# Kernel tuning notes

Hardware: AMD Instinct MI355X
Metric: run time of the kernel (lower is better)

## Reference

```python
import jax, jax.numpy as jnp
import numpy as np

B, S, QS, KS, F, H = 4, 2048, 512, 1024, 1024, 16
DH = F // H  # head dim = 64


def setup_inputs() -> dict:
    key = jax.random.key(0)
    ks = jax.random.split(key, 7)
    s = 0.02
    return {
        "x": jax.random.normal(ks[0], (B, S, QS), dtype=jnp.float32),
        "y": jax.random.normal(ks[1], (B, S, QS), dtype=jnp.float32),
        "z": jax.random.normal(ks[2], (B, S, KS), dtype=jnp.float32),
        "Wq": jax.random.normal(ks[3], (2 * QS, F), dtype=jnp.float32) * s,
        "Wk": jax.random.normal(ks[4], (KS, F), dtype=jnp.float32) * s,
        "Wv": jax.random.normal(ks[5], (KS, F), dtype=jnp.float32) * s,
        "Wo": jax.random.normal(ks[6], (F, F), dtype=jnp.float32) * s,
    }


def _split_heads(t):
    # [B, S, F] -> [B, H, S, DH]
    return t.reshape(B, S, H, DH).transpose(0, 2, 1, 3)


def reference(x, y, z, Wq, Wk, Wv, Wo):
    q = _split_heads(jnp.concatenate([x, y], axis=-1) @ Wq)  # [B,H,S,DH]
    k = _split_heads(z @ Wk)
    v = _split_heads(z @ Wv)
    scale = 1.0 / jnp.sqrt(jnp.asarray(DH, dtype=q.dtype))
    scores = jnp.einsum("bhsd,bhtd->bhst", q, k) * scale  # [B,H,S,S]
    attn = jax.nn.softmax(scores, axis=-1)
    out = jnp.einsum("bhst,bhtd->bhsd", attn, v)  # [B,H,S,DH]
    out = out.transpose(0, 2, 1, 3).reshape(B, S, F)
    return out @ Wo
```

## Files before the change

### kernel.cpp

```cpp
#include <hip/hip_runtime.h>

typedef __attribute__((ext_vector_type(8))) short short8;
typedef __attribute__((ext_vector_type(4))) float f32x4;
typedef __attribute__((ext_vector_type(16))) float f32x16;
typedef __attribute__((ext_vector_type(4))) unsigned short us4;
typedef __attribute__((ext_vector_type(4))) unsigned int u32x4;

#define GLOAD16(gsrc, ldst)                                             \
  __builtin_amdgcn_global_load_lds(                                     \
      (const __attribute__((address_space(1))) unsigned int*)(gsrc),    \
      (__attribute__((address_space(3))) unsigned int*)(ldst), 16, 0, 0)

#define VMEM_DRAIN_BARRIER()                              \
  do {                                                    \
    asm volatile("s_waitcnt vmcnt(0)" ::: "memory");      \
    __builtin_amdgcn_sched_barrier(0);                    \
    __syncthreads();                                      \
  } while (0)

#if __has_builtin(__builtin_amdgcn_exp2f)
#define EXP2F(x) __builtin_amdgcn_exp2f(x)
#else
#define EXP2F(x) exp2f(x)
#endif

static __device__ __forceinline__ unsigned short f2bf(float f) {
  unsigned int u = __float_as_uint(f);
  u += 0x7fffu + ((u >> 16) & 1u);
  return (unsigned short)(u >> 16);
}

static __device__ __forceinline__ unsigned cvtpk(float lo, float hi) {
  unsigned r;
  asm("v_cvt_pk_bf16_f32 %0, %1, %2" : "=v"(r) : "v"(lo), "v"(hi));
  return r;
}

__global__ __launch_bounds__(256) void prep(const float* __restrict__ x,
                                            const float* __restrict__ y,
                                            const float* __restrict__ z,
                                            const float* __restrict__ Wq,
                                            const float* __restrict__ Wk,
                                            const float* __restrict__ Wv,
                                            const float* __restrict__ Wo,
                                            unsigned short* __restrict__ XY,
                                            unsigned short* __restrict__ Z,
                                            unsigned short* __restrict__ WqT,
                                            unsigned short* __restrict__ WkT,
                                            unsigned short* __restrict__ WvT,
                                            unsigned short* __restrict__ WoT) {
  __shared__ __align__(16) unsigned short LT[64 * 72];
  const int bid = blockIdx.x, t = threadIdx.x;

  if (bid < 2048) {
    const int NX = (8192 * 512) / 4;
    const int NZ = (8192 * 1024) / 4;
    const int total = 2 * NX + NZ;
    for (int idx = bid * 256 + t; idx < total; idx += 2048 * 256) {
      const float* src;
      unsigned short* dst;
      if (idx < NX) {
        int p = idx * 4; int row = p >> 9, c = p & 511;
        src = x + p; dst = XY + (size_t)row * 1024 + c;
      } else if (idx < 2 * NX) {
        int p = (idx - NX) * 4; int row = p >> 9, c = p & 511;
        src = y + p; dst = XY + (size_t)row * 1024 + 512 + c;
      } else {
        int p = (idx - 2 * NX) * 4;
        src = z + p; dst = Z + p;
      }
      float4 v = *(const float4*)src;
      us4 o; o[0] = f2bf(v.x); o[1] = f2bf(v.y); o[2] = f2bf(v.z); o[3] = f2bf(v.w);
      *(us4*)dst = o;
    }
    return;
  }

  const int seg = (bid - 2048) >> 8;
  const int local = (bid - 2048) & 255;
  const float* W = (seg == 0) ? Wq : (seg == 1) ? Wk : (seg == 2) ? Wv : Wo;
  unsigned short* WT = (seg == 0) ? WqT : (seg == 1) ? WkT : (seg == 2) ? WvT : WoT;
  const int k0 = (local >> 4) * 64, n0 = (local & 15) * 64;
#pragma unroll
  for (int j = 0; j < 4; ++j) {
    int r = j * 16 + (t >> 4);
    int c = (t & 15) * 4;
    float4 w = *(const float4*)(W + (size_t)(k0 + r) * 1024 + n0 + c);
    LT[(c + 0) * 72 + r] = f2bf(w.x);
    LT[(c + 1) * 72 + r] = f2bf(w.y);
    LT[(c + 2) * 72 + r] = f2bf(w.z);
    LT[(c + 3) * 72 + r] = f2bf(w.w);
  }
  __syncthreads();
#pragma unroll
  for (int j = 0; j < 2; ++j) {
    int n = j * 32 + (t >> 3), ch = t & 7;
    *(short8*)(WT + (size_t)(n0 + n) * 1024 + k0 + ch * 8) =
        *(const short8*)(LT + n * 72 + ch * 8);
  }
}

__global__ __launch_bounds__(256) void qkv_gemm(const unsigned short* __restrict__ XY,
                                                const unsigned short* __restrict__ Zb,
                                                const unsigned short* __restrict__ WqT,
                                                const unsigned short* __restrict__ WkT,
                                                const unsigned short* __restrict__ WvT,
                                                unsigned short* __restrict__ Qb,
                                                unsigned short* __restrict__ Kb,
                                                unsigned short* __restrict__ Vb) {
  __shared__ __align__(16) unsigned short As[128 * 32];
  __shared__ __align__(16) unsigned short Bs[128 * 32];
  const int tid = threadIdx.x;
  const int lane = tid & 63, wid = tid >> 6;
  const int lq = lane & 15, lg = lane >> 4;
  const int wr = wid >> 1, wc = wid & 1;
  const int seg = blockIdx.x >> 3;
  const int m0 = blockIdx.y * 128, n0 = (blockIdx.x & 7) * 128;

  const unsigned short* A;
  const unsigned short* Bt;
  unsigned short* C;
  float scale;
  if (seg == 0)      { A = XY; Bt = WqT; C = Qb; scale = 0.18033688011112042f; }
  else if (seg == 1) { A = Zb; Bt = WkT; C = Kb; scale = 1.0f; }
  else               { A = Zb; Bt = WvT; C = Vb; scale = 1.0f; }

  const int sr = tid >> 2, sc = tid & 3;
  f32x4 acc[4][4] = {};

  for (int k0 = 0; k0 < 1024; k0 += 32) {
    __syncthreads();
#pragma unroll
    for (int i = 0; i < 2; ++i) {
      int r = i * 64 + sr;
      int c = sc ^ ((r >> 1) & 3);
      GLOAD16(A + (size_t)(m0 + r) * 1024 + k0 + c * 8, (char*)As + wid * 1024 + i * 4096);
      GLOAD16(Bt + (size_t)(n0 + r) * 1024 + k0 + c * 8, (char*)Bs + wid * 1024 + i * 4096);
    }
    VMEM_DRAIN_BARRIER();
    short8 af[4], bfr[4];
#pragma unroll
    for (int mf = 0; mf < 4; ++mf) {
      int r = wr * 64 + mf * 16 + lq;
      int c = lg ^ ((r >> 1) & 3);
      af[mf] = *(const short8*)(As + r * 32 + c * 8);
    }
#pragma unroll
    for (int nf = 0; nf < 4; ++nf) {
      int r = wc * 64 + nf * 16 + lq;
      int c = lg ^ ((r >> 1) & 3);
      bfr[nf] = *(const short8*)(Bs + r * 32 + c * 8);
    }
#pragma unroll
    for (int mf = 0; mf < 4; ++mf)
#pragma unroll
      for (int nf = 0; nf < 4; ++nf)
        acc[mf][nf] = __builtin_amdgcn_mfma_f32_16x16x32_bf16(af[mf], bfr[nf],
                                                              acc[mf][nf], 0, 0, 0);
  }

#pragma unroll
  for (int mf = 0; mf < 4; ++mf)
#pragma unroll
    for (int nf = 0; nf < 4; ++nf)
#pragma unroll
      for (int j = 0; j < 4; ++j) {
        int row = m0 + wr * 64 + mf * 16 + lg * 4 + j;
        int col = n0 + wc * 64 + nf * 16 + lq;
        C[(size_t)row * 1024 + col] = f2bf(acc[mf][nf][j] * scale);
      }
}

__global__ __launch_bounds__(256) void gemm_nt(const unsigned short* __restrict__ A,
                                               const unsigned short* __restrict__ Bt,
                                               float* __restrict__ Cout) {
  __shared__ __align__(16) unsigned short As[128 * 32];
  __shared__ __align__(16) unsigned short Bs[128 * 32];
  const int tid = threadIdx.x;
  const int lane = tid & 63, wid = tid >> 6;
  const int lq = lane & 15, lg = lane >> 4;
  const int wr = wid >> 1, wc = wid & 1;
  const int m0 = blockIdx.y * 128, n0 = blockIdx.x * 128;
  const int sr = tid >> 2, sc = tid & 3;

  f32x4 acc[4][4] = {};

  for (int k0 = 0; k0 < 1024; k0 += 32) {
    __syncthreads();
#pragma unroll
    for (int i = 0; i < 2; ++i) {
      int r = i * 64 + sr;
      int c = sc ^ ((r >> 1) & 3);
      GLOAD16(A + (size_t)(m0 + r) * 1024 + k0 + c * 8, (char*)As + wid * 1024 + i * 4096);
      GLOAD16(Bt + (size_t)(n0 + r) * 1024 + k0 + c * 8, (char*)Bs + wid * 1024 + i * 4096);
    }
    VMEM_DRAIN_BARRIER();
    short8 af[4], bfr[4];
#pragma unroll
    for (int mf = 0; mf < 4; ++mf) {
      int r = wr * 64 + mf * 16 + lq;
      int c = lg ^ ((r >> 1) & 3);
      af[mf] = *(const short8*)(As + r * 32 + c * 8);
    }
#pragma unroll
    for (int nf = 0; nf < 4; ++nf) {
      int r = wc * 64 + nf * 16 + lq;
      int c = lg ^ ((r >> 1) & 3);
      bfr[nf] = *(const short8*)(Bs + r * 32 + c * 8);
    }
#pragma unroll
    for (int mf = 0; mf < 4; ++mf)
#pragma unroll
      for (int nf = 0; nf < 4; ++nf)
        acc[mf][nf] = __builtin_amdgcn_mfma_f32_16x16x32_bf16(af[mf], bfr[nf],
                                                              acc[mf][nf], 0, 0, 0);
  }

#pragma unroll
  for (int mf = 0; mf < 4; ++mf)
#pragma unroll
    for (int nf = 0; nf < 4; ++nf)
#pragma unroll
      for (int j = 0; j < 4; ++j) {
        int row = m0 + wr * 64 + mf * 16 + lg * 4 + j;
        int col = n0 + wc * 64 + nf * 16 + lq;
        Cout[(size_t)row * 1024 + col] = acc[mf][nf][j];
      }
}

__global__ __launch_bounds__(256) void vtrans(const unsigned short* __restrict__ V,
                                              unsigned short* __restrict__ Vt) {
  __shared__ __align__(16) unsigned short LT[64 * 72];
  const int bh = blockIdx.y, b = bh >> 4, h = bh & 15;
  const int s0 = blockIdx.x * 64;
  const int t = threadIdx.x;
#pragma unroll
  for (int i = 0; i < 2; ++i) {
    int r = i * 32 + (t >> 3);
    int c = t & 7;
    short8 v = *(const short8*)(V + (size_t)(b * 2048 + s0 + r) * 1024 + h * 64 + c * 8);
#pragma unroll
    for (int e = 0; e < 8; ++e)
      LT[(c * 8 + e) * 72 + r] = (unsigned short)v[e];
  }
  __syncthreads();
#pragma unroll
  for (int i = 0; i < 2; ++i) {
    int d = i * 32 + (t >> 3);
    int c = t & 7;
    *(short8*)(Vt + ((size_t)bh * 64 + d) * 2048 + s0 + c * 8) =
        *(const short8*)(LT + d * 72 + c * 8);
  }
}

__global__ __launch_bounds__(256, 4) void attn6(const unsigned short* __restrict__ Q,
                                                const unsigned short* __restrict__ K,
                                                const unsigned short* __restrict__ Vt,
                                                unsigned short* __restrict__ AO) {
  __shared__ __align__(16) unsigned short Ks[2][64 * 64];
  __shared__ __align__(16) unsigned short Vs[2][64 * 64];

  const int bh = blockIdx.y, b = bh >> 4, h = bh & 15;
  const int q0 = blockIdx.x * 128;
  const int tid = threadIdx.x, lane = tid & 63, w = tid >> 6;
  const int l31 = lane & 31, hi = lane >> 5;
  const int swz = l31 & 7;

  short8 qf[4];
#pragma unroll
  for (int dblk = 0; dblk < 4; ++dblk)
    qf[dblk] = *(const short8*)(Q + (size_t)(b * 2048 + q0 + w * 32 + l31) * 1024 +
                                h * 64 + dblk * 16 + hi * 8);

  short8 ones;
#pragma unroll
  for (int e = 0; e < 8; ++e) ones[e] = (short)0x3F80;

#define STAGE(bf, t)                                                               \
  do {                                                                             \
    _Pragma("unroll")                                                              \
    for (int i = 0; i < 2; ++i) {                                                  \
      int ch = i * 256 + tid;                                                      \
      int r = ch >> 3, c = ch & 7, g = c ^ (r & 7);                                \
      GLOAD16(K + (size_t)(b * 2048 + (t) * 64 + r) * 1024 + h * 64 + g * 8,       \
              (char*)Ks[bf] + i * 4096 + w * 1024);                                \
    }                                                                              \
    _Pragma("unroll")                                                              \
    for (int i = 0; i < 2; ++i) {                                                  \
      int ch = i * 256 + tid;                                                      \
      int r = ch >> 3, c = ch & 7, g = c ^ (r & 7);                                \
      GLOAD16(Vt + ((size_t)bh * 64 + r) * 2048 + (t) * 64 + g * 8,                \
              (char*)Vs[bf] + i * 4096 + w * 1024);                                \
    }                                                                              \
  } while (0)

  STAGE(0, 0);
  VMEM_DRAIN_BARRIER();

  f32x16 od[2] = {};
  f32x16 sums = {};
  int buf = 0;

  for (int t = 0; t < 32; ++t) {
    if (t < 31) STAGE(buf ^ 1, t + 1);

    f32x16 st[2];
    __builtin_amdgcn_s_setprio(1);
#pragma unroll
    for (int kh = 0; kh < 2; ++kh) {
      f32x16 a = {};
#pragma unroll
      for (int dblk = 0; dblk < 4; ++dblk) {
        short8 kf = *(const short8*)(Ks[buf] + (kh * 32 + l31) * 64 +
                                     (((dblk * 2 + hi) ^ swz) * 8));
        a = __builtin_amdgcn_mfma_f32_32x32x16_bf16(kf, qf[dblk], a, 0, 0, 0);
      }
      st[kh] = a;
    }
    __builtin_amdgcn_s_setprio(0);

#pragma unroll
    for (int kh = 0; kh < 2; ++kh)
#pragma unroll
      for (int r = 0; r < 16; ++r) st[kh][r] = EXP2F(st[kh][r]);

    __builtin_amdgcn_s_setprio(1);
#pragma unroll
    for (int ks = 0; ks < 4; ++ks) {
      const int tt = ks >> 1, cm = (ks & 1) * 2;
      unsigned a_lo = cvtpk(st[tt][cm * 4 + 0], st[tt][cm * 4 + 1]);
      unsigned a_hi = cvtpk(st[tt][cm * 4 + 2], st[tt][cm * 4 + 3]);
      unsigned b_lo = cvtpk(st[tt][cm * 4 + 4], st[tt][cm * 4 + 5]);
      unsigned b_hi = cvtpk(st[tt][cm * 4 + 6], st[tt][cm * 4 + 7]);
      auto Xlo = __builtin_amdgcn_permlane32_swap(a_lo, b_lo, false, false);
      auto Xhi = __builtin_amdgcn_permlane32_swap(a_hi, b_hi, false, false);
      u32x4 up;
      up[0] = Xlo[0];
      up[1] = Xhi[0];
      up[2] = Xlo[1];
      up[3] = Xhi[1];
      short8 pa = __builtin_bit_cast(short8, up);
      sums = __builtin_amdgcn_mfma_f32_32x32x16_bf16(ones, pa, sums, 0, 0, 0);
#pragma unroll
      for (int td = 0; td < 2; ++td) {
        short8 vf = *(const short8*)(Vs[buf] + (td * 32 + l31) * 64 +
                                     (((ks * 2 + hi) ^ swz) * 8));
        od[td] = __builtin_amdgcn_mfma_f32_32x32x16_bf16(vf, pa, od[td], 0, 0, 0);
      }
    }
    __builtin_amdgcn_s_setprio(0);

    VMEM_DRAIN_BARRIER();
    buf ^= 1;
  }

  float inv = 1.0f / sums[0];
  const size_t orow = (size_t)(b * 2048 + q0 + w * 32 + l31);
#pragma unroll
  for (int td = 0; td < 2; ++td)
#pragma unroll
    for (int rh = 0; rh < 4; ++rh) {
      us4 o4;
#pragma unroll
      for (int rl = 0; rl < 4; ++rl) o4[rl] = f2bf(od[td][rh * 4 + rl] * inv);
      *(us4*)(AO + orow * 1024 + h * 64 + td * 32 + rh * 8 + hi * 4) = o4;
    }
#undef STAGE
}

extern "C" void kernel_launch(void* const* d_in, const int* in_sizes, int n_in,
                              void* d_out, int out_size, void* d_ws, size_t ws_size,
                              hipStream_t stream) {
  const float* x = (const float*)d_in[0];
  const float* y = (const float*)d_in[1];
  const float* z = (const float*)d_in[2];
  const float* Wq = (const float*)d_in[3];
  const float* Wk = (const float*)d_in[4];
  const float* Wv = (const float*)d_in[5];
  const float* Wo = (const float*)d_in[6];

  char* ws = (char*)d_ws;
  unsigned short* XY  = (unsigned short*)(ws + 0);
  unsigned short* Zb  = (unsigned short*)(ws + 16777216);
  unsigned short* WqT = (unsigned short*)(ws + 33554432);
  unsigned short* WkT = (unsigned short*)(ws + 35651584);
  unsigned short* WvT = (unsigned short*)(ws + 37748736);
  unsigned short* WoT = (unsigned short*)(ws + 39845888);
  unsigned short* Qb  = (unsigned short*)(ws + 41943040);
  unsigned short* Kb  = (unsigned short*)(ws + 58720256);
  unsigned short* Vb  = (unsigned short*)(ws + 75497472);
  unsigned short* Vtg = (unsigned short*)(ws + 92274688);
  unsigned short* AO  = (unsigned short*)(ws + 109051904);

  prep<<<3072, 256, 0, stream>>>(x, y, z, Wq, Wk, Wv, Wo,
                                 XY, Zb, WqT, WkT, WvT, WoT);

  qkv_gemm<<<dim3(24, 64), 256, 0, stream>>>(XY, Zb, WqT, WkT, WvT, Qb, Kb, Vb);

  vtrans<<<dim3(32, 64), 256, 0, stream>>>(Vb, Vtg);
  attn6<<<dim3(16, 64), 256, 0, stream>>>(Qb, Kb, Vtg, AO);

  gemm_nt<<<dim3(8, 64), 256, 0, stream>>>(AO, WoT, (float*)d_out);
}
```

Measured before the change: 217.8 us.

## Double-buffer GEMM LDS tiles and remap attention blocks to XCDs

Both GEMM kernels now use two LDS buffers. The next K-tile is fetched with global_load_lds while MFMAs run on the current tile, which hides global load latency behind compute instead of draining before each step. The attention kernel remaps its linear block index so that all query blocks of a given batch-head land on the same XCD, improving L2 reuse of K/V. The cost is twice the LDS in the GEMMs, which may reduce occupancy.

```diff
diff --git a/kernel.cpp b/kernel.cpp
--- a/kernel.cpp
+++ b/kernel.cpp
@@ -108,8 +108,8 @@
                                                 unsigned short* __restrict__ Qb,
                                                 unsigned short* __restrict__ Kb,
                                                 unsigned short* __restrict__ Vb) {
-  __shared__ __align__(16) unsigned short As[128 * 32];
-  __shared__ __align__(16) unsigned short Bs[128 * 32];
+  __shared__ __align__(16) unsigned short As[2][128 * 32];
+  __shared__ __align__(16) unsigned short Bs[2][128 * 32];
   const int tid = threadIdx.x;
   const int lane = tid & 63, wid = tid >> 6;
   const int lq = lane & 15, lg = lane >> 4;
@@ -126,30 +126,39 @@
   else               { A = Zb; Bt = WvT; C = Vb; scale = 1.0f; }
 
   const int sr = tid >> 2, sc = tid & 3;
+
+#define GSTAGE(bf, kk)                                                       \
+  do {                                                                       \
+    _Pragma("unroll")                                                        \
+    for (int i = 0; i < 2; ++i) {                                            \
+      int r = i * 64 + sr;                                                   \
+      int c = sc ^ ((r >> 1) & 3);                                           \
+      GLOAD16(A + (size_t)(m0 + r) * 1024 + (kk) + c * 8,                    \
+              (char*)As[bf] + wid * 1024 + i * 4096);                        \
+      GLOAD16(Bt + (size_t)(n0 + r) * 1024 + (kk) + c * 8,                   \
+              (char*)Bs[bf] + wid * 1024 + i * 4096);                        \
+    }                                                                        \
+  } while (0)
+
   f32x4 acc[4][4] = {};
+  GSTAGE(0, 0);
+  VMEM_DRAIN_BARRIER();
+  int buf = 0;
 
   for (int k0 = 0; k0 < 1024; k0 += 32) {
-    __syncthreads();
-#pragma unroll
-    for (int i = 0; i < 2; ++i) {
-      int r = i * 64 + sr;
-      int c = sc ^ ((r >> 1) & 3);
-      GLOAD16(A + (size_t)(m0 + r) * 1024 + k0 + c * 8, (char*)As + wid * 1024 + i * 4096);
-      GLOAD16(Bt + (size_t)(n0 + r) * 1024 + k0 + c * 8, (char*)Bs + wid * 1024 + i * 4096);
-    }
-    VMEM_DRAIN_BARRIER();
+    if (k0 + 32 < 1024) GSTAGE(buf ^ 1, k0 + 32);
     short8 af[4], bfr[4];
 #pragma unroll
     for (int mf = 0; mf < 4; ++mf) {
       int r = wr * 64 + mf * 16 + lq;
       int c = lg ^ ((r >> 1) & 3);
-      af[mf] = *(const short8*)(As + r * 32 + c * 8);
+      af[mf] = *(const short8*)(As[buf] + r * 32 + c * 8);
     }
 #pragma unroll
     for (int nf = 0; nf < 4; ++nf) {
       int r = wc * 64 + nf * 16 + lq;
       int c = lg ^ ((r >> 1) & 3);
-      bfr[nf] = *(const short8*)(Bs + r * 32 + c * 8);
+      bfr[nf] = *(const short8*)(Bs[buf] + r * 32 + c * 8);
     }
 #pragma unroll
     for (int mf = 0; mf < 4; ++mf)
@@ -157,7 +166,10 @@
       for (int nf = 0; nf < 4; ++nf)
         acc[mf][nf] = __builtin_amdgcn_mfma_f32_16x16x32_bf16(af[mf], bfr[nf],
                                                               acc[mf][nf], 0, 0, 0);
-  }
+    VMEM_DRAIN_BARRIER();
+    buf ^= 1;
+  }
+#undef GSTAGE
 
 #pragma unroll
   for (int mf = 0; mf < 4; ++mf)
@@ -174,8 +186,8 @@
 __global__ __launch_bounds__(256) void gemm_nt(const unsigned short* __restrict__ A,
                                                const unsigned short* __restrict__ Bt,
                                                float* __restrict__ Cout) {
-  __shared__ __align__(16) unsigned short As[128 * 32];
-  __shared__ __align__(16) unsigned short Bs[128 * 32];
+  __shared__ __align__(16) unsigned short As[2][128 * 32];
+  __shared__ __align__(16) unsigned short Bs[2][128 * 32];
   const int tid = threadIdx.x;
   const int lane = tid & 63, wid = tid >> 6;
   const int lq = lane & 15, lg = lane >> 4;
@@ -183,30 +195,38 @@
   const int m0 = blockIdx.y * 128, n0 = blockIdx.x * 128;
   const int sr = tid >> 2, sc = tid & 3;
 
+#define GSTAGE(bf, kk)                                                       \
+  do {                                                                       \
+    _Pragma("unroll")                                                        \
+    for (int i = 0; i < 2; ++i) {                                            \
+      int r = i * 64 + sr;                                                   \
+      int c = sc ^ ((r >> 1) & 3);                                           \
+      GLOAD16(A + (size_t)(m0 + r) * 1024 + (kk) + c * 8,                    \
+              (char*)As[bf] + wid * 1024 + i * 4096);                        \
+      GLOAD16(Bt + (size_t)(n0 + r) * 1024 + (kk) + c * 8,                   \
+              (char*)Bs[bf] + wid * 1024 + i * 4096);                        \
+    }                                                                        \
+  } while (0)
+
   f32x4 acc[4][4] = {};
+  GSTAGE(0, 0);
+  VMEM_DRAIN_BARRIER();
+  int buf = 0;
 
   for (int k0 = 0; k0 < 1024; k0 += 32) {
-    __syncthreads();
-#pragma unroll
-    for (int i = 0; i < 2; ++i) {
-      int r = i * 64 + sr;
-      int c = sc ^ ((r >> 1) & 3);
-      GLOAD16(A + (size_t)(m0 + r) * 1024 + k0 + c * 8, (char*)As + wid * 1024 + i * 4096);
-      GLOAD16(Bt + (size_t)(n0 + r) * 1024 + k0 + c * 8, (char*)Bs + wid * 1024 + i * 4096);
-    }
-    VMEM_DRAIN_BARRIER();
+    if (k0 + 32 < 1024) GSTAGE(buf ^ 1, k0 + 32);
     short8 af[4], bfr[4];
 #pragma unroll
     for (int mf = 0; mf < 4; ++mf) {
       int r = wr * 64 + mf * 16 + lq;
       int c = lg ^ ((r >> 1) & 3);
-      af[mf] = *(const short8*)(As + r * 32 + c * 8);
+      af[mf] = *(const short8*)(As[buf] + r * 32 + c * 8);
     }
 #pragma unroll
     for (int nf = 0; nf < 4; ++nf) {
       int r = wc * 64 + nf * 16 + lq;
       int c = lg ^ ((r >> 1) & 3);
-      bfr[nf] = *(const short8*)(Bs + r * 32 + c * 8);
+      bfr[nf] = *(const short8*)(Bs[buf] + r * 32 + c * 8);
     }
 #pragma unroll
     for (int mf = 0; mf < 4; ++mf)
@@ -214,7 +234,10 @@
       for (int nf = 0; nf < 4; ++nf)
         acc[mf][nf] = __builtin_amdgcn_mfma_f32_16x16x32_bf16(af[mf], bfr[nf],
                                                               acc[mf][nf], 0, 0, 0);
-  }
+    VMEM_DRAIN_BARRIER();
+    buf ^= 1;
+  }
+#undef GSTAGE
 
 #pragma unroll
   for (int mf = 0; mf < 4; ++mf)
@@ -253,15 +276,19 @@
   }
 }
 
-__global__ __launch_bounds__(256, 4) void attn6(const unsigned short* __restrict__ Q,
+__global__ __launch_bounds__(256, 4) void attn7(const unsigned short* __restrict__ Q,
                                                 const unsigned short* __restrict__ K,
                                                 const unsigned short* __restrict__ Vt,
                                                 unsigned short* __restrict__ AO) {
   __shared__ __align__(16) unsigned short Ks[2][64 * 64];
   __shared__ __align__(16) unsigned short Vs[2][64 * 64];
 
-  const int bh = blockIdx.y, b = bh >> 4, h = bh & 15;
-  const int q0 = blockIdx.x * 128;
+  const int lin = blockIdx.x + (blockIdx.y << 4);
+  const int xcd = lin & 7, rest = lin >> 3;
+  const int bh = xcd * 8 + (rest >> 4);
+  const int q0 = (rest & 15) * 128;
+  const int b = bh >> 4, h = bh & 15;
+
   const int tid = threadIdx.x, lane = tid & 63, w = tid >> 6;
   const int l31 = lane & 31, hi = lane >> 5;
   const int swz = l31 & 7;
@@ -398,7 +425,7 @@
   qkv_gemm<<<dim3(24, 64), 256, 0, stream>>>(XY, Zb, WqT, WkT, WvT, Qb, Kb, Vb);
 
   vtrans<<<dim3(32, 64), 256, 0, stream>>>(Vb, Vtg);
-  attn6<<<dim3(16, 64), 256, 0, stream>>>(Qb, Kb, Vtg, AO);
+  attn7<<<dim3(16, 64), 256, 0, stream>>>(Qb, Kb, Vtg, AO);
 
   gemm_nt<<<dim3(8, 64), 256, 0, stream>>>(AO, WoT, (float*)d_out);
 }
```

New measurement: 223.6 us. 2.7% more time.
